# Performance work log

Measured on AMD Instinct MI355X. Metric: run time of the kernel, lower is better.

Reference implementation:

```python
import jax, jax.numpy as jnp
import numpy as np

# ---- static config (matches torch module defaults) ----
SPATIAL = np.array([[100, 100], [50, 50], [25, 25], [13, 13]], dtype=np.int64)  # [L,2] (H,W)
EMBED, HEADS, LEVELS, POINTS = 256, 8, 4, 4
HEAD_DIM = EMBED // HEADS
TOTAL_POINTS = HEADS * LEVELS * POINTS
BS, LQ = 32, 300
LV = int((SPATIAL[:, 0] * SPATIAL[:, 1]).sum())  # 13294


def setup_inputs() -> dict:
    key = jax.random.key(0)
    ks = jax.random.split(key, 12)
    s = 1.0 / np.sqrt(EMBED)
    return {
        "query": jax.random.normal(ks[0], (BS, LQ, EMBED), jnp.float32),
        "reference_points": jax.random.uniform(ks[1], (BS, LQ, LEVELS, 2), jnp.float32),
        "value": jax.random.normal(ks[2], (BS, LV, EMBED), jnp.float32),
        "value_spatial_shapes": jnp.asarray(SPATIAL),
        # learned parameters (torch: Linear weight [out,in] -> stored here as [in,out])
        "W_off": jax.random.normal(ks[3], (EMBED, TOTAL_POINTS * 2), jnp.float32) * 0.01,
        "b_off": jax.random.normal(ks[4], (TOTAL_POINTS * 2,), jnp.float32) * 0.01,
        "W_attn": jax.random.normal(ks[5], (EMBED, TOTAL_POINTS), jnp.float32) * s,
        "b_attn": jnp.zeros((TOTAL_POINTS,), jnp.float32),
        "W_val": jax.random.normal(ks[6], (EMBED, EMBED), jnp.float32) * s,
        "b_val": jnp.zeros((EMBED,), jnp.float32),
        "W_out": jax.random.normal(ks[7], (EMBED, EMBED), jnp.float32) * s,
        "b_out": jnp.zeros((EMBED,), jnp.float32),
    }


def _bilinear_sample(v, grid, H, W):
    """F.grid_sample(mode='bilinear', padding_mode='zeros', align_corners=False).
    v: [H*W, c], grid: [Lq, P, 2] in [-1, 1] (x, y). Returns [Lq, P, c]."""
    x = (grid[..., 0] + 1.0) * 0.5 * W - 0.5
    y = (grid[..., 1] + 1.0) * 0.5 * H - 0.5
    x0f, y0f = jnp.floor(x), jnp.floor(y)
    lx, ly = x - x0f, y - y0f
    x0, y0 = x0f.astype(jnp.int32), y0f.astype(jnp.int32)

    def gather(iy, ix):
        valid = ((iy >= 0) & (iy < H) & (ix >= 0) & (ix < W)).astype(v.dtype)[..., None]
        idx = jnp.clip(iy, 0, H - 1) * W + jnp.clip(ix, 0, W - 1)
        return v[idx] * valid

    return (gather(y0, x0) * ((1 - ly) * (1 - lx))[..., None]
            + gather(y0, x0 + 1) * ((1 - ly) * lx)[..., None]
            + gather(y0 + 1, x0) * (ly * (1 - lx))[..., None]
            + gather(y0 + 1, x0 + 1) * (ly * lx)[..., None])


def _ms_deform_attn_core(value, sampling_grids, attention_weights):
    """value: [bs, Lv, H, c]; sampling_grids: [bs, Lq, H, L, P, 2] in [-1,1];
    attention_weights: [bs, Lq, H, L, P] -> output [bs, Lq, H*c]."""
    bs, Lq = sampling_grids.shape[:2]
    samples = []
    start = 0
    for lvl in range(LEVELS):
        H, W = int(SPATIAL[lvl, 0]), int(SPATIAL[lvl, 1])
        # [bs, HW, nh, c] -> [bs*nh, HW, c]
        v_l = value[:, start:start + H * W]
        v_l = v_l.transpose(0, 2, 1, 3).reshape(bs * HEADS, H * W, HEAD_DIM)
        # [bs, Lq, nh, P, 2] -> [bs*nh, Lq, P, 2]
        g_l = sampling_grids[:, :, :, lvl].transpose(0, 2, 1, 3, 4).reshape(bs * HEADS, Lq, POINTS, 2)
        samples.append(jax.vmap(lambda vv, gg: _bilinear_sample(vv, gg, H, W))(v_l, g_l))
        start += H * W
    stacked = jnp.stack(samples, axis=2)  # [bs*nh, Lq, L, P, c]
    aw = attention_weights.transpose(0, 2, 1, 3, 4).reshape(bs * HEADS, Lq, LEVELS, POINTS)
    out = (stacked * aw[..., None]).sum(axis=(2, 3))  # [bs*nh, Lq, c]
    return out.reshape(bs, HEADS, Lq, HEAD_DIM).transpose(0, 2, 1, 3).reshape(bs, Lq, EMBED)


def reference(query, reference_points, value, value_spatial_shapes,
              W_off, b_off, W_attn, b_attn, W_val, b_val, W_out, b_out):
    bs, Lq = query.shape[:2]
    Lv = value.shape[1]

    value_p = (value @ W_val + b_val).reshape(bs, Lv, HEADS, HEAD_DIM)

    offsets = (query @ W_off + b_off).reshape(bs, Lq, HEADS, LEVELS, POINTS, 2)
    attn = jax.nn.softmax((query @ W_attn + b_attn).reshape(bs, Lq, HEADS, LEVELS * POINTS), axis=-1)
    attn = attn.reshape(bs, Lq, HEADS, LEVELS, POINTS)

    # offset_normalizer = flip(spatial_shapes) -> (W, H) per level
    norm = jnp.asarray(SPATIAL[:, ::-1].copy(), jnp.float32)  # [L, 2]
    sampling_locations = (reference_points[:, :, None, :, None, :]
                          + offsets / norm[None, None, None, :, None, :])
    sampling_grids = 2.0 * sampling_locations - 1.0

    out = _ms_deform_attn_core(value_p, sampling_grids, attn)
    return out @ W_out + b_out
```

## Files before the change

kernel.cpp:

```cpp
#include <hip/hip_runtime.h>
#include <hip/hip_bf16.h>

#define BS_   32
#define LQ_   300
#define LV_   13294
#define EMBED_ 256
#define HEADS_ 8
#define HEAD_DIM_ 32
#define NCHUNK_ 13294
#define PSTRIDE_ 512

typedef __attribute__((ext_vector_type(8))) short bf16x8;
typedef __attribute__((ext_vector_type(4))) float f32x4;

__device__ inline short f2bf(float f) {
  union { float f; unsigned u; } x; x.f = f;
  return (short)((x.u + 0x7FFF + ((x.u >> 16) & 1)) >> 16);
}
__device__ inline short f2bf_i(float f) {
  union { __hip_bfloat16 h; short s; } u;
  u.h = __float2bfloat16(f);
  return u.s;
}
__device__ inline float bf2f(short s) {
  union { unsigned u; float f; } x; x.u = ((unsigned)(unsigned short)s) << 16;
  return x.f;
}

__device__ __forceinline__ void gld_lds16(const void* g, void* l) {
  __builtin_amdgcn_global_load_lds(
      (const __attribute__((address_space(1))) unsigned int*)g,
      (__attribute__((address_space(3))) unsigned int*)l, 16, 0, 0);
}

__global__ void convert_all(const float* __restrict__ W_off,
                            const float* __restrict__ W_attn,
                            const float* __restrict__ W_val,
                            const float* __restrict__ W_out,
                            short* __restrict__ WtQ,
                            short* __restrict__ WtV,
                            short* __restrict__ WtO) {
  const int n = blockIdx.x;
  const int k = threadIdx.x;
  if (n < 384) {
    WtQ[n * 256 + k] = (n < 256) ? f2bf(W_off[k * 256 + n])
                                 : f2bf(W_attn[k * 128 + (n - 256)]);
  } else if (n < 640) {
    WtV[(n - 384) * 256 + k] = f2bf(W_val[k * 256 + (n - 384)]);
  } else {
    WtO[(n - 640) * 256 + k] = f2bf(W_out[k * 256 + (n - 640)]);
  }
}

__global__ __launch_bounds__(512, 2) void mega_gemm(
    const float* __restrict__ value, const short* __restrict__ WtV,
    const float* __restrict__ b_val, short* __restrict__ Vp,
    const float* __restrict__ query, const short* __restrict__ WtQ,
    const float* __restrict__ b_off, const float* __restrict__ b_attn,
    float* __restrict__ offs, float* __restrict__ logits) {
  __shared__ float As[16384];

  const int tid = threadIdx.x;
  const int lane = tid & 63;
  const int w = tid >> 6;
  const int lr = lane & 15;
  const int lkq = lane >> 4;
  const int bid = blockIdx.x;

  if (bid < 150) {
    const size_t m0 = (size_t)bid * 64;
#pragma unroll
    for (int i = 0; i < 8; ++i) {
      const int row = w * 8 + i;
      gld_lds16(query + (m0 + row) * 256 + ((lane ^ (row & 7)) * 4), As + row * 256);
    }
    __syncthreads();

    if (w < 6) {
      const int n0 = w * 64;
      f32x4 acc[4][4];
#pragma unroll
      for (int i = 0; i < 4; ++i)
#pragma unroll
        for (int jj = 0; jj < 4; ++jj) acc[i][jj] = (f32x4){0.f, 0.f, 0.f, 0.f};

#pragma unroll
      for (int kt = 0; kt < 8; ++kt) {
        bf16x8 bfr[4];
#pragma unroll
        for (int nf = 0; nf < 4; ++nf)
          bfr[nf] = *(const bf16x8*)(WtQ + (size_t)(n0 + nf * 16 + lr) * 256 + kt * 32 + lkq * 8);
#pragma unroll
        for (int mf = 0; mf < 4; ++mf) {
          const int row = mf * 16 + lr;
          const int g = kt * 8 + lkq * 2;
          const f32x4 a0 = *(const f32x4*)(As + row * 256 + (((g    ) ^ (row & 7)) * 4));
          const f32x4 a1 = *(const f32x4*)(As + row * 256 + (((g + 1) ^ (row & 7)) * 4));
          bf16x8 af;
#pragma unroll
          for (int i = 0; i < 4; ++i) {
            af[i]     = f2bf_i(a0[i]);
            af[i + 4] = f2bf_i(a1[i]);
          }
#pragma unroll
          for (int nf = 0; nf < 4; ++nf)
            acc[mf][nf] = __builtin_amdgcn_mfma_f32_16x16x32_bf16(af, bfr[nf], acc[mf][nf], 0, 0, 0);
        }
      }

      float bv[4];
#pragma unroll
      for (int nf = 0; nf < 4; ++nf) {
        const int n = n0 + nf * 16 + lr;
        bv[nf] = (n < 256) ? b_off[n] : b_attn[n - 256];
      }
      const int lq4 = lkq * 4;
#pragma unroll
      for (int mf = 0; mf < 4; ++mf)
#pragma unroll
        for (int r = 0; r < 4; ++r) {
          const size_t m = m0 + mf * 16 + lq4 + r;
#pragma unroll
          for (int nf = 0; nf < 4; ++nf) {
            const int n = n0 + nf * 16 + lr;
            const float v = acc[mf][nf][r] + bv[nf];
            if (n < 256) offs[m * 256 + n] = v;
            else         logits[m * 128 + (n - 256)] = v;
          }
        }
    }
    __syncthreads();
  }

  bf16x8 bfr[2][8];
#pragma unroll
  for (int nf = 0; nf < 2; ++nf) {
    const size_t bbase = (size_t)(w * 32 + nf * 16 + lr) * 256 + lkq * 8;
#pragma unroll
    for (int kt = 0; kt < 8; ++kt)
      bfr[nf][kt] = *(const bf16x8*)(WtV + bbase + kt * 32);
  }
  float bv[2];
#pragma unroll
  for (int nf = 0; nf < 2; ++nf) bv[nf] = b_val[w * 32 + nf * 16 + lr];

  auto stage = [&](int buf, int c) {
    const float* src = value + (size_t)c * (32 * 256);
#pragma unroll
    for (int i = 0; i < 4; ++i) {
      const int r = w * 4 + i;
      gld_lds16(src + r * 256 + ((lane ^ (r & 7)) * 4), As + buf * 8192 + r * 256);
    }
  };

  const int c0 = bid;
  stage(0, c0);
  asm volatile("s_waitcnt vmcnt(0)" ::: "memory");
  __syncthreads();

  int cb = 0;
  for (int c = c0; c < NCHUNK_; c += PSTRIDE_) {
    const int nxt = c + PSTRIDE_;
    if (nxt < NCHUNK_) stage(cb ^ 1, nxt);

    f32x4 acc[2][2];
#pragma unroll
    for (int i = 0; i < 2; ++i)
#pragma unroll
      for (int jj = 0; jj < 2; ++jj) acc[i][jj] = (f32x4){0.f, 0.f, 0.f, 0.f};

    const float* as = As + cb * 8192;
#pragma unroll
    for (int kt = 0; kt < 8; ++kt) {
      const int r0 = lr;
      const int r1 = 16 + lr;
      const int g = kt * 8 + lkq * 2;
      const f32x4 a00 = *(const f32x4*)(as + r0 * 256 + (((g    ) ^ (r0 & 7)) * 4));
      const f32x4 a01 = *(const f32x4*)(as + r0 * 256 + (((g + 1) ^ (r0 & 7)) * 4));
      const f32x4 a10 = *(const f32x4*)(as + r1 * 256 + (((g    ) ^ (r1 & 7)) * 4));
      const f32x4 a11 = *(const f32x4*)(as + r1 * 256 + (((g + 1) ^ (r1 & 7)) * 4));
      bf16x8 af0, af1;
#pragma unroll
      for (int i = 0; i < 4; ++i) {
        af0[i]     = f2bf_i(a00[i]);
        af0[i + 4] = f2bf_i(a01[i]);
        af1[i]     = f2bf_i(a10[i]);
        af1[i + 4] = f2bf_i(a11[i]);
      }
      acc[0][0] = __builtin_amdgcn_mfma_f32_16x16x32_bf16(af0, bfr[0][kt], acc[0][0], 0, 0, 0);
      acc[0][1] = __builtin_amdgcn_mfma_f32_16x16x32_bf16(af0, bfr[1][kt], acc[0][1], 0, 0, 0);
      acc[1][0] = __builtin_amdgcn_mfma_f32_16x16x32_bf16(af1, bfr[0][kt], acc[1][0], 0, 0, 0);
      acc[1][1] = __builtin_amdgcn_mfma_f32_16x16x32_bf16(af1, bfr[1][kt], acc[1][1], 0, 0, 0);
    }

#pragma unroll
    for (int mf = 0; mf < 2; ++mf)
#pragma unroll
      for (int rr = 0; rr < 4; ++rr) {
        const unsigned m = (unsigned)c * 32 + mf * 16 + lkq * 4 + rr;
        const unsigned b_ = m / LV_;
        const unsigned pos = m - b_ * LV_;
        const size_t rowbase = ((size_t)(b_ * HEADS_ + w) * LV_ + pos) * HEAD_DIM_;
#pragma unroll
        for (int nf = 0; nf < 2; ++nf)
          Vp[rowbase + nf * 16 + lr] = f2bf(acc[mf][nf][rr] + bv[nf]);
      }

    if (nxt < NCHUNK_) {
      asm volatile("s_waitcnt vmcnt(16)" ::: "memory");
      asm volatile("s_barrier" ::: "memory");
    }
    cb ^= 1;
  }
}

__global__ __launch_bounds__(256, 2) void gemm_qproj(
    const float* __restrict__ A, const short* __restrict__ Wt,
    const float* __restrict__ bias, float* __restrict__ C) {
  __shared__ float As[64 * 256];

  const int tid = threadIdx.x;
  const int lane = tid & 63;
  const int w = tid >> 6;
  const int n0 = w * 64;
  const size_t m0 = (size_t)blockIdx.x * 64;
  const int lr = lane & 15;
  const int lkq = lane >> 4;

#pragma unroll
  for (int i = 0; i < 16; ++i) {
    const int row = w * 16 + i;
    gld_lds16(A + (m0 + row) * 256 + ((lane ^ (row & 7)) * 4), As + row * 256);
  }

  bf16x8 bfr[4][8];
#pragma unroll
  for (int nf = 0; nf < 4; ++nf) {
    const size_t bbase = (size_t)(n0 + nf * 16 + lr) * 256 + lkq * 8;
#pragma unroll
    for (int kt = 0; kt < 8; ++kt)
      bfr[nf][kt] = *(const bf16x8*)(Wt + bbase + kt * 32);
  }

  f32x4 acc[4][4];
#pragma unroll
  for (int i = 0; i < 4; ++i)
#pragma unroll
    for (int jj = 0; jj < 4; ++jj) acc[i][jj] = (f32x4){0.f, 0.f, 0.f, 0.f};

  __syncthreads();

#pragma unroll
  for (int kt = 0; kt < 8; ++kt) {
#pragma unroll
    for (int mf = 0; mf < 4; ++mf) {
      const int row = mf * 16 + lr;
      const int gbase = kt * 8 + lkq * 2;
      const f32x4 a0 = *(const f32x4*)(As + row * 256 + ((gbase) ^ (row & 7)) * 4);
      const f32x4 a1 = *(const f32x4*)(As + row * 256 + ((gbase + 1) ^ (row & 7)) * 4);
      bf16x8 af;
#pragma unroll
      for (int i = 0; i < 4; ++i) {
        af[i]     = f2bf_i(a0[i]);
        af[i + 4] = f2bf_i(a1[i]);
      }
#pragma unroll
      for (int nf = 0; nf < 4; ++nf)
        acc[mf][nf] = __builtin_amdgcn_mfma_f32_16x16x32_bf16(af, bfr[nf][kt], acc[mf][nf], 0, 0, 0);
    }
  }

  float bv[4];
#pragma unroll
  for (int nf = 0; nf < 4; ++nf) bv[nf] = bias[n0 + nf * 16 + lr];
  const int lq4 = lkq * 4;
#pragma unroll
  for (int mf = 0; mf < 4; ++mf)
#pragma unroll
    for (int r = 0; r < 4; ++r) {
      const size_t m = m0 + mf * 16 + lq4 + r;
#pragma unroll
      for (int nf = 0; nf < 4; ++nf) {
        const int n = n0 + nf * 16 + lr;
        C[m * 256 + n] = acc[mf][nf][r] + bv[nf];
      }
    }
}

__global__ __launch_bounds__(256) void msda_sample_fused(
    const float* __restrict__ ref_pts,
    const float* __restrict__ offsets,
    const float* __restrict__ logits,
    const short* __restrict__ value_p,
    float* __restrict__ tmp)
{
  const int t = blockIdx.x * 256 + threadIdx.x;
  const int c8 = t & 3;
  const int h = (t >> 2) & 7;
  const int row = t >> 5;
  const int b = row / LQ_;

  const int HS[4] = {100, 50, 25, 13};
  const int START[4] = {0, 10000, 12500, 13125};

  const float* lg = logits + (size_t)row * 128 + h * 16;
  float wv[16];
  float mx = -1e30f;
#pragma unroll
  for (int i = 0; i < 4; ++i) {
    const f32x4 v = *(const f32x4*)(lg + i * 4);
#pragma unroll
    for (int jj = 0; jj < 4; ++jj) { wv[i * 4 + jj] = v[jj]; mx = fmaxf(mx, v[jj]); }
  }
  float sum = 0.f;
#pragma unroll
  for (int i = 0; i < 16; ++i) { wv[i] = __expf(wv[i] - mx); sum += wv[i]; }
  const float inv = 1.0f / sum;
#pragma unroll
  for (int i = 0; i < 16; ++i) wv[i] *= inv;

  const float* offr = offsets + (size_t)row * 256 + h * 32;
  const float* refr = ref_pts + (size_t)row * 8;

  float acc[8];
#pragma unroll
  for (int jj = 0; jj < 8; ++jj) acc[jj] = 0.f;

#pragma unroll
  for (int l = 0; l < 4; ++l) {
    const int HH = HS[l];
    const int WW = HS[l];
    const float fH = (float)HH, fW = (float)WW;
    const float rx = refr[l * 2 + 0];
    const float ry = refr[l * 2 + 1];
    const short* vbase =
        value_p + ((size_t)(b * HEADS_ + h) * LV_ + START[l]) * HEAD_DIM_ + c8 * 8;
#pragma unroll
    for (int p = 0; p < 4; ++p) {
      const float ox = offr[(l * 4 + p) * 2 + 0];
      const float oy = offr[(l * 4 + p) * 2 + 1];
      const float x = (rx + ox / fW) * fW - 0.5f;
      const float y = (ry + oy / fH) * fH - 0.5f;
      const float x0f = floorf(x), y0f = floorf(y);
      const float fx = x - x0f, fy = y - y0f;
      const int x0 = (int)x0f, y0 = (int)y0f;
      const float wgt = wv[l * 4 + p];
      const float iy0 = (y0 >= 0 && y0 < HH) ? 1.f : 0.f;
      const float iy1 = (y0 + 1 >= 0 && y0 + 1 < HH) ? 1.f : 0.f;
      const float ix0 = (x0 >= 0 && x0 < WW) ? 1.f : 0.f;
      const float ix1 = (x0 + 1 >= 0 && x0 + 1 < WW) ? 1.f : 0.f;
      const float w00 = (1.f - fy) * (1.f - fx) * wgt * iy0 * ix0;
      const float w01 = (1.f - fy) * fx * wgt * iy0 * ix1;
      const float w10 = fy * (1.f - fx) * wgt * iy1 * ix0;
      const float w11 = fy * fx * wgt * iy1 * ix1;
      const int xc0 = min(max(x0, 0), WW - 1);
      const int xc1 = min(max(x0 + 1, 0), WW - 1);
      const int yc0 = min(max(y0, 0), HH - 1);
      const int yc1 = min(max(y0 + 1, 0), HH - 1);
      const bf16x8 q00 = *(const bf16x8*)(vbase + (size_t)(yc0 * WW + xc0) * HEAD_DIM_);
      const bf16x8 q01 = *(const bf16x8*)(vbase + (size_t)(yc0 * WW + xc1) * HEAD_DIM_);
      const bf16x8 q10 = *(const bf16x8*)(vbase + (size_t)(yc1 * WW + xc0) * HEAD_DIM_);
      const bf16x8 q11 = *(const bf16x8*)(vbase + (size_t)(yc1 * WW + xc1) * HEAD_DIM_);
#pragma unroll
      for (int jj = 0; jj < 8; ++jj) {
        acc[jj] += w00 * bf2f(q00[jj]) + w01 * bf2f(q01[jj]) +
                   w10 * bf2f(q10[jj]) + w11 * bf2f(q11[jj]);
      }
    }
  }
  float* o = tmp + (size_t)row * 256 + h * 32 + c8 * 8;
  f32x4 o0 = {acc[0], acc[1], acc[2], acc[3]};
  f32x4 o1 = {acc[4], acc[5], acc[6], acc[7]};
  *(f32x4*)(o) = o0;
  *(f32x4*)(o + 4) = o1;
}

extern "C" void kernel_launch(void* const* d_in, const int* in_sizes, int n_in,
                              void* d_out, int out_size, void* d_ws, size_t ws_size,
                              hipStream_t stream) {
  const float* query  = (const float*)d_in[0];
  const float* refpts = (const float*)d_in[1];
  const float* value  = (const float*)d_in[2];
  const float* W_off  = (const float*)d_in[4];
  const float* b_off  = (const float*)d_in[5];
  const float* W_attn = (const float*)d_in[6];
  const float* b_attn = (const float*)d_in[7];
  const float* W_val  = (const float*)d_in[8];
  const float* b_val  = (const float*)d_in[9];
  const float* W_out  = (const float*)d_in[10];
  const float* b_out  = (const float*)d_in[11];
  float* out = (float*)d_out;

  char* ws = (char*)d_ws;
  short* value_p = (short*)ws;
  size_t off = (size_t)BS_ * HEADS_ * LV_ * HEAD_DIM_ * 2;
  float* offsets = (float*)(ws + off); off += (size_t)BS_ * LQ_ * 256 * 4;
  float* logits  = (float*)(ws + off); off += (size_t)BS_ * LQ_ * 128 * 4;
  float* tmp     = (float*)(ws + off); off += (size_t)BS_ * LQ_ * 256 * 4;
  short* WtQ = (short*)(ws + off); off += 384 * 256 * 2;
  short* WtV = (short*)(ws + off); off += 256 * 256 * 2;
  short* WtO = (short*)(ws + off); off += 256 * 256 * 2;

  const int MQ = BS_ * LQ_;

  convert_all<<<896, 256, 0, stream>>>(W_off, W_attn, W_val, W_out, WtQ, WtV, WtO);
  mega_gemm<<<PSTRIDE_, 512, 0, stream>>>(value, WtV, b_val, value_p,
                                          query, WtQ, b_off, b_attn, offsets, logits);
  msda_sample_fused<<<(MQ * 32) / 256, 256, 0, stream>>>(refpts, offsets, logits, value_p, tmp);
  gemm_qproj<<<MQ / 64, 256, 0, stream>>>(tmp, WtO, b_out, out);
}
```

Measured before the change: 206.3 us.

## Use 16-row chunks with a 4-buffer, two-ahead prefetch pipeline in value projection

The value-projection kernel now processes 16-row chunks instead of 32-row chunks and keeps four LDS buffers, staging two chunks ahead of the one being computed. Hand-tuned s_waitcnt vmcnt counts replace the previous single-ahead double-buffer wait. The goal is to hide global load latency behind compute for this memory-bound GEMM, at the cost of smaller MFMA work per iteration and more loop overhead. The vmcnt values depend on the exact number of outstanding loads and stores, including the Vp stores, so the ordering is fragile.

```diff
diff --git a/kernel.cpp b/kernel.cpp
--- a/kernel.cpp
+++ b/kernel.cpp
@@ -7,7 +7,7 @@
 #define EMBED_ 256
 #define HEADS_ 8
 #define HEAD_DIM_ 32
-#define NCHUNK_ 13294
+#define NCHUNK16_ 26588
 #define PSTRIDE_ 512
 
 typedef __attribute__((ext_vector_type(8))) short bf16x8;
@@ -140,77 +140,62 @@
     for (int kt = 0; kt < 8; ++kt)
       bfr[nf][kt] = *(const bf16x8*)(WtV + bbase + kt * 32);
   }
-  float bv[2];
-#pragma unroll
-  for (int nf = 0; nf < 2; ++nf) bv[nf] = b_val[w * 32 + nf * 16 + lr];
-
-  auto stage = [&](int buf, int c) {
-    const float* src = value + (size_t)c * (32 * 256);
-#pragma unroll
-    for (int i = 0; i < 4; ++i) {
-      const int r = w * 4 + i;
-      gld_lds16(src + r * 256 + ((lane ^ (r & 7)) * 4), As + buf * 8192 + r * 256);
+  float bv0 = b_val[w * 32 + lr];
+  float bv1 = b_val[w * 32 + 16 + lr];
+
+  auto stage16 = [&](int buf, int c) {
+    const float* src = value + (size_t)c * (16 * 256);
+#pragma unroll
+    for (int i = 0; i < 2; ++i) {
+      const int r = w * 2 + i;
+      gld_lds16(src + r * 256 + ((lane ^ (r & 7)) * 4), As + buf * 4096 + r * 256);
     }
   };
 
   const int c0 = bid;
-  stage(0, c0);
-  asm volatile("s_waitcnt vmcnt(0)" ::: "memory");
-  __syncthreads();
-
-  int cb = 0;
-  for (int c = c0; c < NCHUNK_; c += PSTRIDE_) {
-    const int nxt = c + PSTRIDE_;
-    if (nxt < NCHUNK_) stage(cb ^ 1, nxt);
-
-    f32x4 acc[2][2];
-#pragma unroll
-    for (int i = 0; i < 2; ++i)
-#pragma unroll
-      for (int jj = 0; jj < 2; ++jj) acc[i][jj] = (f32x4){0.f, 0.f, 0.f, 0.f};
-
-    const float* as = As + cb * 8192;
+  stage16(0, c0);
+  stage16(1, c0 + PSTRIDE_);
+
+  int it = 0;
+  for (int c = c0; c < NCHUNK16_; c += PSTRIDE_, ++it) {
+    const bool s1 = (c + PSTRIDE_ < NCHUNK16_);
+    const bool s2 = (c + 2 * PSTRIDE_ < NCHUNK16_);
+    if (s2) stage16((it + 2) & 3, c + 2 * PSTRIDE_);
+
+    if (it == 0)      asm volatile("s_waitcnt vmcnt(4)" ::: "memory");
+    else if (it == 1) asm volatile("s_waitcnt vmcnt(12)" ::: "memory");
+    else if (s2)      asm volatile("s_waitcnt vmcnt(20)" ::: "memory");
+    else if (s1)      asm volatile("s_waitcnt vmcnt(18)" ::: "memory");
+    else              asm volatile("s_waitcnt vmcnt(16)" ::: "memory");
+    asm volatile("s_barrier" ::: "memory");
+
+    f32x4 acc0 = (f32x4){0.f, 0.f, 0.f, 0.f};
+    f32x4 acc1 = (f32x4){0.f, 0.f, 0.f, 0.f};
+    const float* as = As + (it & 3) * 4096;
 #pragma unroll
     for (int kt = 0; kt < 8; ++kt) {
-      const int r0 = lr;
-      const int r1 = 16 + lr;
       const int g = kt * 8 + lkq * 2;
-      const f32x4 a00 = *(const f32x4*)(as + r0 * 256 + (((g    ) ^ (r0 & 7)) * 4));
-      const f32x4 a01 = *(const f32x4*)(as + r0 * 256 + (((g + 1) ^ (r0 & 7)) * 4));
-      const f32x4 a10 = *(const f32x4*)(as + r1 * 256 + (((g    ) ^ (r1 & 7)) * 4));
-      const f32x4 a11 = *(const f32x4*)(as + r1 * 256 + (((g + 1) ^ (r1 & 7)) * 4));
-      bf16x8 af0, af1;
+      const f32x4 a0 = *(const f32x4*)(as + lr * 256 + (((g    ) ^ (lr & 7)) * 4));
+      const f32x4 a1 = *(const f32x4*)(as + lr * 256 + (((g + 1) ^ (lr & 7)) * 4));
+      bf16x8 af;
 #pragma unroll
       for (int i = 0; i < 4; ++i) {
-        af0[i]     = f2bf_i(a00[i]);
-        af0[i + 4] = f2bf_i(a01[i]);
-        af1[i]     = f2bf_i(a10[i]);
-        af1[i + 4] = f2bf_i(a11[i]);
-      }
-      acc[0][0] = __builtin_amdgcn_mfma_f32_16x16x32_bf16(af0, bfr[0][kt], acc[0][0], 0, 0, 0);
-      acc[0][1] = __builtin_amdgcn_mfma_f32_16x16x32_bf16(af0, bfr[1][kt], acc[0][1], 0, 0, 0);
-      acc[1][0] = __builtin_amdgcn_mfma_f32_16x16x32_bf16(af1, bfr[0][kt], acc[1][0], 0, 0, 0);
-      acc[1][1] = __builtin_amdgcn_mfma_f32_16x16x32_bf16(af1, bfr[1][kt], acc[1][1], 0, 0, 0);
-    }
-
-#pragma unroll
-    for (int mf = 0; mf < 2; ++mf)
-#pragma unroll
-      for (int rr = 0; rr < 4; ++rr) {
-        const unsigned m = (unsigned)c * 32 + mf * 16 + lkq * 4 + rr;
-        const unsigned b_ = m / LV_;
-        const unsigned pos = m - b_ * LV_;
-        const size_t rowbase = ((size_t)(b_ * HEADS_ + w) * LV_ + pos) * HEAD_DIM_;
-#pragma unroll
-        for (int nf = 0; nf < 2; ++nf)
-          Vp[rowbase + nf * 16 + lr] = f2bf(acc[mf][nf][rr] + bv[nf]);
-      }
-
-    if (nxt < NCHUNK_) {
-      asm volatile("s_waitcnt vmcnt(16)" ::: "memory");
-      asm volatile("s_barrier" ::: "memory");
-    }
-    cb ^= 1;
+        af[i]     = f2bf_i(a0[i]);
+        af[i + 4] = f2bf_i(a1[i]);
+      }
+      acc0 = __builtin_amdgcn_mfma_f32_16x16x32_bf16(af, bfr[0][kt], acc0, 0, 0, 0);
+      acc1 = __builtin_amdgcn_mfma_f32_16x16x32_bf16(af, bfr[1][kt], acc1, 0, 0, 0);
+    }
+
+#pragma unroll
+    for (int rr = 0; rr < 4; ++rr) {
+      const unsigned m = (unsigned)c * 16 + lkq * 4 + rr;
+      const unsigned b_ = m / LV_;
+      const unsigned pos = m - b_ * LV_;
+      const size_t rowbase = ((size_t)(b_ * HEADS_ + w) * LV_ + pos) * HEAD_DIM_;
+      Vp[rowbase + lr]      = f2bf(acc0[rr] + bv0);
+      Vp[rowbase + 16 + lr] = f2bf(acc1[rr] + bv1);
+    }
   }
 }
 
```

Measured after the change: 214.6 us. 4.0% more time.

## Halve waves per block in mega_gemm, widen each wave to two heads

Applied to the files above, without the earlier changes.

The fused projection kernel now launches 256 threads per block instead of 512. Each wave computes 64 value-projection columns (two heads), so every LDS-loaded and converted A fragment feeds twice as many MFMAs. The query projection is split across 300 blocks, with one group doing offset columns and another doing attention-logit columns. The trade-off is higher register pressure (128 VGPRs of resident weights) and fewer waves per CU to hide global load latency.

```diff
diff --git a/kernel.cpp b/kernel.cpp
--- a/kernel.cpp
+++ b/kernel.cpp
@@ -52,7 +52,7 @@
   }
 }
 
-__global__ __launch_bounds__(512, 2) void mega_gemm(
+__global__ __launch_bounds__(256, 2) void mega_gemm(
     const float* __restrict__ value, const short* __restrict__ WtV,
     const float* __restrict__ b_val, short* __restrict__ Vp,
     const float* __restrict__ query, const short* __restrict__ WtQ,
@@ -67,17 +67,19 @@
   const int lkq = lane >> 4;
   const int bid = blockIdx.x;
 
-  if (bid < 150) {
-    const size_t m0 = (size_t)bid * 64;
-#pragma unroll
-    for (int i = 0; i < 8; ++i) {
-      const int row = w * 8 + i;
+  if (bid < 300) {
+    const bool typeA = (bid < 150);
+    const int tile = typeA ? bid : bid - 150;
+    const size_t m0 = (size_t)tile * 64;
+#pragma unroll
+    for (int i = 0; i < 16; ++i) {
+      const int row = w * 16 + i;
       gld_lds16(query + (m0 + row) * 256 + ((lane ^ (row & 7)) * 4), As + row * 256);
     }
     __syncthreads();
 
-    if (w < 6) {
-      const int n0 = w * 64;
+    if (typeA || w < 2) {
+      const int n0g = typeA ? (w * 64) : (256 + w * 64);
       f32x4 acc[4][4];
 #pragma unroll
       for (int i = 0; i < 4; ++i)
@@ -86,10 +88,10 @@
 
 #pragma unroll
       for (int kt = 0; kt < 8; ++kt) {
-        bf16x8 bfr[4];
+        bf16x8 bq[4];
 #pragma unroll
         for (int nf = 0; nf < 4; ++nf)
-          bfr[nf] = *(const bf16x8*)(WtQ + (size_t)(n0 + nf * 16 + lr) * 256 + kt * 32 + lkq * 8);
+          bq[nf] = *(const bf16x8*)(WtQ + (size_t)(n0g + nf * 16 + lr) * 256 + kt * 32 + lkq * 8);
 #pragma unroll
         for (int mf = 0; mf < 4; ++mf) {
           const int row = mf * 16 + lr;
@@ -104,15 +106,15 @@
           }
 #pragma unroll
           for (int nf = 0; nf < 4; ++nf)
-            acc[mf][nf] = __builtin_amdgcn_mfma_f32_16x16x32_bf16(af, bfr[nf], acc[mf][nf], 0, 0, 0);
+            acc[mf][nf] = __builtin_amdgcn_mfma_f32_16x16x32_bf16(af, bq[nf], acc[mf][nf], 0, 0, 0);
         }
       }
 
-      float bv[4];
+      float bvq[4];
 #pragma unroll
       for (int nf = 0; nf < 4; ++nf) {
-        const int n = n0 + nf * 16 + lr;
-        bv[nf] = (n < 256) ? b_off[n] : b_attn[n - 256];
+        const int n = n0g + nf * 16 + lr;
+        bvq[nf] = (n < 256) ? b_off[n] : b_attn[n - 256];
       }
       const int lq4 = lkq * 4;
 #pragma unroll
@@ -122,8 +124,8 @@
           const size_t m = m0 + mf * 16 + lq4 + r;
 #pragma unroll
           for (int nf = 0; nf < 4; ++nf) {
-            const int n = n0 + nf * 16 + lr;
-            const float v = acc[mf][nf][r] + bv[nf];
+            const int n = n0g + nf * 16 + lr;
+            const float v = acc[mf][nf][r] + bvq[nf];
             if (n < 256) offs[m * 256 + n] = v;
             else         logits[m * 128 + (n - 256)] = v;
           }
@@ -132,23 +134,23 @@
     __syncthreads();
   }
 
-  bf16x8 bfr[2][8];
-#pragma unroll
-  for (int nf = 0; nf < 2; ++nf) {
-    const size_t bbase = (size_t)(w * 32 + nf * 16 + lr) * 256 + lkq * 8;
+  bf16x8 bfr[4][8];
+#pragma unroll
+  for (int nf = 0; nf < 4; ++nf) {
+    const size_t bbase = (size_t)(w * 64 + nf * 16 + lr) * 256 + lkq * 8;
 #pragma unroll
     for (int kt = 0; kt < 8; ++kt)
       bfr[nf][kt] = *(const bf16x8*)(WtV + bbase + kt * 32);
   }
-  float bv[2];
-#pragma unroll
-  for (int nf = 0; nf < 2; ++nf) bv[nf] = b_val[w * 32 + nf * 16 + lr];
+  float bv[4];
+#pragma unroll
+  for (int nf = 0; nf < 4; ++nf) bv[nf] = b_val[w * 64 + nf * 16 + lr];
 
   auto stage = [&](int buf, int c) {
     const float* src = value + (size_t)c * (32 * 256);
 #pragma unroll
-    for (int i = 0; i < 4; ++i) {
-      const int r = w * 4 + i;
+    for (int i = 0; i < 8; ++i) {
+      const int r = w * 8 + i;
       gld_lds16(src + r * 256 + ((lane ^ (r & 7)) * 4), As + buf * 8192 + r * 256);
     }
   };
@@ -163,11 +165,11 @@
     const int nxt = c + PSTRIDE_;
     if (nxt < NCHUNK_) stage(cb ^ 1, nxt);
 
-    f32x4 acc[2][2];
+    f32x4 acc[2][4];
 #pragma unroll
     for (int i = 0; i < 2; ++i)
 #pragma unroll
-      for (int jj = 0; jj < 2; ++jj) acc[i][jj] = (f32x4){0.f, 0.f, 0.f, 0.f};
+      for (int jj = 0; jj < 4; ++jj) acc[i][jj] = (f32x4){0.f, 0.f, 0.f, 0.f};
 
     const float* as = As + cb * 8192;
 #pragma unroll
@@ -187,10 +189,11 @@
         af1[i]     = f2bf_i(a10[i]);
         af1[i + 4] = f2bf_i(a11[i]);
       }
-      acc[0][0] = __builtin_amdgcn_mfma_f32_16x16x32_bf16(af0, bfr[0][kt], acc[0][0], 0, 0, 0);
-      acc[0][1] = __builtin_amdgcn_mfma_f32_16x16x32_bf16(af0, bfr[1][kt], acc[0][1], 0, 0, 0);
-      acc[1][0] = __builtin_amdgcn_mfma_f32_16x16x32_bf16(af1, bfr[0][kt], acc[1][0], 0, 0, 0);
-      acc[1][1] = __builtin_amdgcn_mfma_f32_16x16x32_bf16(af1, bfr[1][kt], acc[1][1], 0, 0, 0);
+#pragma unroll
+      for (int nf = 0; nf < 4; ++nf) {
+        acc[0][nf] = __builtin_amdgcn_mfma_f32_16x16x32_bf16(af0, bfr[nf][kt], acc[0][nf], 0, 0, 0);
+        acc[1][nf] = __builtin_amdgcn_mfma_f32_16x16x32_bf16(af1, bfr[nf][kt], acc[1][nf], 0, 0, 0);
+      }
     }
 
 #pragma unroll
@@ -200,14 +203,16 @@
         const unsigned m = (unsigned)c * 32 + mf * 16 + lkq * 4 + rr;
         const unsigned b_ = m / LV_;
         const unsigned pos = m - b_ * LV_;
-        const size_t rowbase = ((size_t)(b_ * HEADS_ + w) * LV_ + pos) * HEAD_DIM_;
-#pragma unroll
-        for (int nf = 0; nf < 2; ++nf)
-          Vp[rowbase + nf * 16 + lr] = f2bf(acc[mf][nf][rr] + bv[nf]);
+        const size_t rb0 = ((size_t)(b_ * HEADS_ + 2 * w) * LV_ + pos) * HEAD_DIM_;
+        const size_t rb1 = rb0 + (size_t)LV_ * HEAD_DIM_;
+        Vp[rb0 + lr]      = f2bf(acc[mf][0][rr] + bv[0]);
+        Vp[rb0 + 16 + lr] = f2bf(acc[mf][1][rr] + bv[1]);
+        Vp[rb1 + lr]      = f2bf(acc[mf][2][rr] + bv[2]);
+        Vp[rb1 + 16 + lr] = f2bf(acc[mf][3][rr] + bv[3]);
       }
 
     if (nxt < NCHUNK_) {
-      asm volatile("s_waitcnt vmcnt(16)" ::: "memory");
+      asm volatile("s_waitcnt vmcnt(32)" ::: "memory");
       asm volatile("s_barrier" ::: "memory");
     }
     cb ^= 1;
@@ -404,7 +409,7 @@
   const int MQ = BS_ * LQ_;
 
   convert_all<<<896, 256, 0, stream>>>(W_off, W_attn, W_val, W_out, WtQ, WtV, WtO);
-  mega_gemm<<<PSTRIDE_, 512, 0, stream>>>(value, WtV, b_val, value_p,
+  mega_gemm<<<PSTRIDE_, 256, 0, stream>>>(value, WtV, b_val, value_p,
                                           query, WtQ, b_off, b_attn, offsets, logits);
   msda_sample_fused<<<(MQ * 32) / 256, 256, 0, stream>>>(refpts, offsets, logits, value_p, tmp);
   gemm_qproj<<<MQ / 64, 256, 0, stream>>>(tmp, WtO, b_out, out);
```

Measured after the change: 206.0 us. No clear change (-0.1%).
